# Kernel tuning notes

Measured on AMD Instinct MI355X. Metric: run time of the kernel, lower is better.

Reference implementation:

```python
import jax, jax.numpy as jnp
import numpy as np

B, N, D_IN, D, E, HEADS = 64, 512, 33, 32, 8192, 4
L, K_HOP, FF = 2, 2, 64  # num_layers, k_hop, dim_feedforward=2*d_out


def setup_inputs():
    key = jax.random.key(0)
    ks = iter(jax.random.split(key, 40))
    def nrm(shape, s=0.05):
        return jax.random.normal(next(ks), shape, jnp.float32) * s
    return {
        "H": jax.random.normal(next(ks), (B, N, D_IN), jnp.float32),
        "edge_index": jax.random.randint(next(ks), (2, E), 0, N, jnp.int32),
        # ObsEmbedding: Linear(33,32) ReLU Linear(32,32) ReLU LayerNorm(32)
        "emb_W1": nrm((D_IN, 32)), "emb_b1": jnp.zeros((32,), jnp.float32),
        "emb_W2": nrm((32, 32)), "emb_b2": jnp.zeros((32,), jnp.float32),
        "emb_ln_g": jnp.ones((32,), jnp.float32), "emb_ln_b": jnp.zeros((32,), jnp.float32),
        # per transformer layer: k_hop PNA-style GNN structure extractor
        # each hop: concat(self, mean, max, sum) -> Linear(4D, D), ReLU
        "gnn_W": nrm((L, K_HOP, 4 * D, D)), "gnn_b": jnp.zeros((L, K_HOP, D), jnp.float32),
        # structure-aware attention: Q,K from GNN-extracted features, V from x
        "Wq": nrm((L, D, D)), "Wk": nrm((L, D, D)), "Wv": nrm((L, D, D)), "Wo": nrm((L, D, D)),
        "bn1_g": jnp.ones((L, D), jnp.float32), "bn1_b": jnp.zeros((L, D), jnp.float32),
        "ff_W1": nrm((L, D, FF)), "ff_b1": jnp.zeros((L, FF), jnp.float32),
        "ff_W2": nrm((L, FF, D)), "ff_b2": jnp.zeros((L, D), jnp.float32),
        "bn2_g": jnp.ones((L, D), jnp.float32), "bn2_b": jnp.zeros((L, D), jnp.float32),
        # final node-level head Linear(d_model, num_class=d_out)
        "out_W": nrm((D, D)), "out_b": jnp.zeros((D,), jnp.float32),
    }


def _ln(x, g, b):
    m = x.mean(-1, keepdims=True)
    v = x.var(-1, keepdims=True)
    return (x - m) * jax.lax.rsqrt(v + 1e-5) * g + b


def _bn(x, g, b):  # batch_norm over all nodes of all graphs (training-mode stats)
    m = x.mean((0, 1))
    v = x.var((0, 1))
    return (x - m) * jax.lax.rsqrt(v + 1e-5) * g + b


def reference(H, edge_index, emb_W1, emb_b1, emb_W2, emb_b2, emb_ln_g, emb_ln_b,
              gnn_W, gnn_b, Wq, Wk, Wv, Wo, bn1_g, bn1_b,
              ff_W1, ff_b1, ff_W2, ff_b2, bn2_g, bn2_b, out_W, out_b):
    src, dst = edge_index[0], edge_index[1]
    # ObsEmbedding
    x = jax.nn.relu(H @ emb_W1 + emb_b1)
    x = jax.nn.relu(x @ emb_W2 + emb_b2)
    x = _ln(x, emb_ln_g, emb_ln_b)  # [B,N,D]
    cnt = jnp.zeros((N, 1), x.dtype).at[dst].add(1.0)  # in-degree, shared across batch
    dh = D // HEADS
    inv_sqrt_dh = np.float32(1.0 / np.sqrt(dh))
    for l in range(L):
        # --- k-hop structure extractor (PNA-style multi-aggregator message passing) ---
        h = x
        for k in range(K_HOP):
            msg = h[:, src]                                   # [B,E,D] gather
            s = jnp.zeros_like(h).at[:, dst].add(msg)         # sum aggregate
            mean = s / jnp.maximum(cnt, 1.0)
            mx = jnp.full_like(h, -1e30).at[:, dst].max(msg)  # max aggregate
            mx = jnp.where(cnt > 0, mx, 0.0)
            h = jax.nn.relu(jnp.concatenate([h, mean, mx, s], -1) @ gnn_W[l, k] + gnn_b[l, k])
        # --- structure-aware multi-head attention (full attention within graph) ---
        q = (h @ Wq[l]).reshape(B, N, HEADS, dh)
        kk = (h @ Wk[l]).reshape(B, N, HEADS, dh)
        v = (x @ Wv[l]).reshape(B, N, HEADS, dh)
        att = jax.nn.softmax(jnp.einsum("bqhd,bkhd->bhqk", q, kk) * inv_sqrt_dh, axis=-1)
        o = jnp.einsum("bhqk,bkhd->bqhd", att, v).reshape(B, N, D) @ Wo[l]
        x = _bn(x + o, bn1_g[l], bn1_b[l])
        f = jax.nn.relu(x @ ff_W1[l] + ff_b1[l]) @ ff_W2[l] + ff_b2[l]
        x = _bn(x + f, bn2_g[l], bn2_b[l])
    return x @ out_W + out_b  # [B,N,d_out], eval mode so dropout is identity
```

## Files before the change

kernel.cpp:

```cpp
#include <hip/hip_runtime.h>
#include <hip/hip_bf16.h>

#define BB 64
#define NN 512
#define DIN 33
#define DD 32
#define EE 8192
#define NHEADS 4
#define DH 8
#define FFD 64

typedef __attribute__((ext_vector_type(4))) float f32x4;
typedef __attribute__((ext_vector_type(4))) short bf16x4;

static __device__ __forceinline__ short f2bf(float x) {
    unsigned u = __float_as_uint(x);
    u = (u + 0x7FFFu + ((u >> 16) & 1u)) >> 16;
    return (short)u;
}

static __device__ __forceinline__ unsigned pack_trunc(float a, float b) {
    return (__float_as_uint(a) >> 16) | (__float_as_uint(b) & 0xFFFF0000u);
}

static __device__ __forceinline__ void mfma16(f32x4& d, bf16x4 a, bf16x4 b) {
#if __has_builtin(__builtin_amdgcn_mfma_f32_16x16x16bf16_1k)
    d = __builtin_amdgcn_mfma_f32_16x16x16bf16_1k(a, b, d, 0, 0, 0);
#else
    asm volatile("s_nop 1\n\tv_mfma_f32_16x16x16_bf16 %0, %1, %2, %0\n\ts_nop 7"
                 : "+v"(d) : "v"(a), "v"(b));
#endif
}

__global__ __launch_bounds__(512) void k_csr(const int* __restrict__ ei,
                                             float* __restrict__ cnt_f,
                                             int* __restrict__ csr_off,
                                             int* __restrict__ csr_src,
                                             float* __restrict__ stats) {
    __shared__ int cnt_s[NN];
    __shared__ int wsum[8];
    int tid = threadIdx.x;
    cnt_s[tid] = 0;
    if (tid < 256) stats[tid] = 0.f;
    __syncthreads();
    const int* src = ei;
    const int* dst = ei + EE;
    for (int e = tid; e < EE; e += 512) atomicAdd(&cnt_s[dst[e]], 1);
    __syncthreads();
    int c = cnt_s[tid];
    int lane = tid & 63, w = tid >> 6;
    int sc_ = c;
    #pragma unroll
    for (int off = 1; off < 64; off <<= 1) {
        int nv = __shfl_up(sc_, off, 64);
        if (lane >= off) sc_ += nv;
    }
    if (lane == 63) wsum[w] = sc_;
    __syncthreads();
    if (tid == 0) {
        int a = 0;
        #pragma unroll
        for (int i = 0; i < 8; ++i) { int t = wsum[i]; wsum[i] = a; a += t; }
    }
    __syncthreads();
    int excl = sc_ - c + wsum[w];
    cnt_f[tid] = (float)c;
    csr_off[tid] = excl;
    if (tid == 511) csr_off[NN] = excl + c;
    __syncthreads();
    cnt_s[tid] = excl;
    __syncthreads();
    for (int e = tid; e < EE; e += 512) {
        int d = dst[e];
        int p = atomicAdd(&cnt_s[d], 1);
        csr_src[p] = src[e];
    }
}

__global__ __launch_bounds__(256) void k_emb(const float* __restrict__ H,
                                             const float* __restrict__ W1, const float* __restrict__ b1,
                                             const float* __restrict__ W2, const float* __restrict__ b2,
                                             const float* __restrict__ g,  const float* __restrict__ be,
                                             float* __restrict__ xb, float* __restrict__ xt) {
    __shared__ float sW1[DIN * DD];
    __shared__ float sW2[DD * DD];
    __shared__ float sb1[DD], sb2[DD], sg[DD], sbe[DD];
    __shared__ float sin_[8][DIN + 3];
    int tid = threadIdx.x;
    for (int i = tid; i < DIN * DD; i += 256) sW1[i] = W1[i];
    for (int i = tid; i < DD * DD; i += 256) sW2[i] = W2[i];
    if (tid < DD) { sb1[tid] = b1[tid]; sb2[tid] = b2[tid]; sg[tid] = g[tid]; sbe[tid] = be[tid]; }
    int grp = tid >> 5, lane = tid & 31;
    size_t node = (size_t)blockIdx.x * 8 + grp;
    const float* hrow = H + node * DIN;
    sin_[grp][lane] = hrow[lane];
    if (lane == 0) sin_[grp][32] = hrow[32];
    __syncthreads();
    float acc = sb1[lane];
    #pragma unroll
    for (int i = 0; i < DIN; ++i) acc += sin_[grp][i] * sW1[i * DD + lane];
    acc = fmaxf(acc, 0.f);
    float acc2 = sb2[lane];
    #pragma unroll
    for (int i = 0; i < DD; ++i) acc2 += __shfl(acc, i, 32) * sW2[i * DD + lane];
    acc2 = fmaxf(acc2, 0.f);
    float s = acc2;
    for (int off = 16; off; off >>= 1) s += __shfl_xor(s, off, 32);
    float m = s * (1.f / 32.f);
    float dv = acc2 - m;
    float sq = dv * dv;
    for (int off = 16; off; off >>= 1) sq += __shfl_xor(sq, off, 32);
    float var = sq * (1.f / 32.f);
    float v = dv * rsqrtf(var + 1e-5f) * sg[lane] + sbe[lane];
    xb[node * DD + lane] = v;
    int b = (int)(node >> 9), n = (int)(node & 511);
    xt[(size_t)n * 2048 + b * DD + lane] = v;
}

__global__ __launch_bounds__(256) void k_gnn1(const float* __restrict__ src, float* __restrict__ ht,
                                              const float* __restrict__ cnt_f,
                                              const int* __restrict__ csr_off,
                                              const int* __restrict__ csr_src,
                                              const float* __restrict__ W, const float* __restrict__ bias,
                                              const float* __restrict__ bnstats,
                                              const float* __restrict__ bng, const float* __restrict__ bnb) {
    __shared__ short conc[32 * 132];
    __shared__ short sWt[32 * 132];
    __shared__ float sb[DD];
    __shared__ float scv[DD], offv[DD];
    int tid = threadIdx.x;
    int n = blockIdx.x >> 1, half = blockIdx.x & 1;
    for (int i = tid; i < 128 * DD; i += 256) {
        int k = i >> 5, d = i & 31;
        sWt[d * 132 + k] = f2bf(W[i]);
    }
    if (tid < DD) {
        sb[tid] = bias[tid];
        if (bnstats) {
            float mean = bnstats[tid] * (1.f / 32768.f);
            float var  = bnstats[DD + tid] * (1.f / 32768.f) - mean * mean;
            float sc = rsqrtf(var + 1e-5f) * bng[tid];
            scv[tid] = sc; offv[tid] = bnb[tid] - mean * sc;
        } else { scv[tid] = 1.f; offv[tid] = 0.f; }
    }
    __syncthreads();
    float4 sc4, of4;
    { int d0 = (tid * 4) & 31;
      sc4.x = scv[d0]; sc4.y = scv[d0 + 1]; sc4.z = scv[d0 + 2]; sc4.w = scv[d0 + 3];
      of4.x = offv[d0]; of4.y = offv[d0 + 1]; of4.z = offv[d0 + 2]; of4.w = offv[d0 + 3]; }
    const float* xbase = src + (size_t)half * 1024 + tid * 4;
    float4 hv = *(const float4*)&xbase[(size_t)n * 2048];
    hv.x = fmaf(hv.x, sc4.x, of4.x); hv.y = fmaf(hv.y, sc4.y, of4.y);
    hv.z = fmaf(hv.z, sc4.z, of4.z); hv.w = fmaf(hv.w, sc4.w, of4.w);
    float4 s = {0.f, 0.f, 0.f, 0.f};
    float4 mx = {-1e30f, -1e30f, -1e30f, -1e30f};
    int beg = csr_off[n], end = csr_off[n + 1];
    int idx = beg;
    for (; idx + 3 < end; idx += 4) {
        int s0 = csr_src[idx], s1 = csr_src[idx + 1], s2 = csr_src[idx + 2], s3 = csr_src[idx + 3];
        float4 v0 = *(const float4*)&xbase[(size_t)s0 * 2048];
        float4 v1 = *(const float4*)&xbase[(size_t)s1 * 2048];
        float4 v2 = *(const float4*)&xbase[(size_t)s2 * 2048];
        float4 v3 = *(const float4*)&xbase[(size_t)s3 * 2048];
        v0.x = fmaf(v0.x, sc4.x, of4.x); v0.y = fmaf(v0.y, sc4.y, of4.y);
        v0.z = fmaf(v0.z, sc4.z, of4.z); v0.w = fmaf(v0.w, sc4.w, of4.w);
        v1.x = fmaf(v1.x, sc4.x, of4.x); v1.y = fmaf(v1.y, sc4.y, of4.y);
        v1.z = fmaf(v1.z, sc4.z, of4.z); v1.w = fmaf(v1.w, sc4.w, of4.w);
        v2.x = fmaf(v2.x, sc4.x, of4.x); v2.y = fmaf(v2.y, sc4.y, of4.y);
        v2.z = fmaf(v2.z, sc4.z, of4.z); v2.w = fmaf(v2.w, sc4.w, of4.w);
        v3.x = fmaf(v3.x, sc4.x, of4.x); v3.y = fmaf(v3.y, sc4.y, of4.y);
        v3.z = fmaf(v3.z, sc4.z, of4.z); v3.w = fmaf(v3.w, sc4.w, of4.w);
        s.x += (v0.x + v1.x) + (v2.x + v3.x);
        s.y += (v0.y + v1.y) + (v2.y + v3.y);
        s.z += (v0.z + v1.z) + (v2.z + v3.z);
        s.w += (v0.w + v1.w) + (v2.w + v3.w);
        mx.x = fmaxf(fmaxf(mx.x, v0.x), fmaxf(v1.x, fmaxf(v2.x, v3.x)));
        mx.y = fmaxf(fmaxf(mx.y, v0.y), fmaxf(v1.y, fmaxf(v2.y, v3.y)));
        mx.z = fmaxf(fmaxf(mx.z, v0.z), fmaxf(v1.z, fmaxf(v2.z, v3.z)));
        mx.w = fmaxf(fmaxf(mx.w, v0.w), fmaxf(v1.w, fmaxf(v2.w, v3.w)));
    }
    for (; idx < end; ++idx) {
        int s0 = csr_src[idx];
        float4 v0 = *(const float4*)&xbase[(size_t)s0 * 2048];
        v0.x = fmaf(v0.x, sc4.x, of4.x); v0.y = fmaf(v0.y, sc4.y, of4.y);
        v0.z = fmaf(v0.z, sc4.z, of4.z); v0.w = fmaf(v0.w, sc4.w, of4.w);
        s.x += v0.x; s.y += v0.y; s.z += v0.z; s.w += v0.w;
        mx.x = fmaxf(mx.x, v0.x); mx.y = fmaxf(mx.y, v0.y);
        mx.z = fmaxf(mx.z, v0.z); mx.w = fmaxf(mx.w, v0.w);
    }
    float c = cnt_f[n];
    float rinv = 1.f / fmaxf(c, 1.f);
    if (!(c > 0.f)) { mx.x = 0.f; mx.y = 0.f; mx.z = 0.f; mx.w = 0.f; }
    int bl = tid >> 3, d0 = (tid & 7) * 4;
    short* cp = &conc[bl * 132];
    bf16x4 t;
    t.x = f2bf(hv.x); t.y = f2bf(hv.y); t.z = f2bf(hv.z); t.w = f2bf(hv.w);
    *(bf16x4*)&cp[d0] = t;
    t.x = f2bf(s.x * rinv); t.y = f2bf(s.y * rinv); t.z = f2bf(s.z * rinv); t.w = f2bf(s.w * rinv);
    *(bf16x4*)&cp[32 + d0] = t;
    t.x = f2bf(mx.x); t.y = f2bf(mx.y); t.z = f2bf(mx.z); t.w = f2bf(mx.w);
    *(bf16x4*)&cp[64 + d0] = t;
    t.x = f2bf(s.x); t.y = f2bf(s.y); t.z = f2bf(s.z); t.w = f2bf(s.w);
    *(bf16x4*)&cp[96 + d0] = t;
    __syncthreads();
    int wid = tid >> 6, lane = tid & 63;
    int cc = lane & 15, g = lane >> 4;
    int arow = (wid >> 1) * 16 + cc;
    int bcol = (wid & 1) * 16 + cc;
    f32x4 acc = {0.f, 0.f, 0.f, 0.f};
    #pragma unroll
    for (int ks = 0; ks < 8; ++ks) {
        bf16x4 af = *(const bf16x4*)&conc[arow * 132 + ks * 16 + g * 4];
        bf16x4 bfr = *(const bf16x4*)&sWt[bcol * 132 + ks * 16 + g * 4];
        mfma16(acc, af, bfr);
    }
    float bia = sb[bcol];
    int brow = (wid >> 1) * 16 + g * 4;
    float* obase = &ht[(size_t)n * 2048 + half * 1024 + bcol];
    #pragma unroll
    for (int r = 0; r < 4; ++r) {
        obase[(size_t)(brow + r) * DD] = fmaxf(acc[r] + bia, 0.f);
    }
}

__global__ __launch_bounds__(256) void k_gnn2(const float* __restrict__ hsrc,
                                              const float* __restrict__ cnt_f,
                                              const int* __restrict__ csr_off,
                                              const int* __restrict__ csr_src,
                                              const float* __restrict__ W, const float* __restrict__ bias,
                                              const float* __restrict__ xsrc,
                                              const float* __restrict__ bnstats,
                                              const float* __restrict__ bng, const float* __restrict__ bnb,
                                              const float* __restrict__ Wq, const float* __restrict__ Wk,
                                              const float* __restrict__ Wv,
                                              short* __restrict__ qb2, short* __restrict__ kb2,
                                              short* __restrict__ vb2) {
    __shared__ short conc[32 * 132];
    __shared__ short sWt[32 * 132];
    __shared__ short sWqT[32 * 36], sWkT[32 * 36], sWvT[32 * 36];
    __shared__ short h_lds[32 * 36], x_lds[32 * 36];
    __shared__ float sb[DD];
    __shared__ float scv[DD], offv[DD];
    int tid = threadIdx.x;
    int n = blockIdx.x >> 1, half = blockIdx.x & 1;
    for (int i = tid; i < 128 * DD; i += 256) {
        int k = i >> 5, d = i & 31;
        sWt[d * 132 + k] = f2bf(W[i]);
    }
    {
        const float isq = 0.35355339059327373f;
        for (int i = tid; i < 1024; i += 256) {
            int k = i >> 5, col = i & 31;
            sWqT[col * 36 + k] = f2bf(Wq[i] * isq);
            sWkT[col * 36 + k] = f2bf(Wk[i]);
            sWvT[col * 36 + k] = f2bf(Wv[i]);
        }
    }
    if (tid < DD) {
        sb[tid] = bias[tid];
        if (bnstats) {
            float mean = bnstats[tid] * (1.f / 32768.f);
            float var  = bnstats[DD + tid] * (1.f / 32768.f) - mean * mean;
            float sc = rsqrtf(var + 1e-5f) * bng[tid];
            scv[tid] = sc; offv[tid] = bnb[tid] - mean * sc;
        } else { scv[tid] = 1.f; offv[tid] = 0.f; }
    }
    __syncthreads();
    {
        int bl = tid >> 3, d0 = (tid & 7) * 4;
        float4 x4 = *(const float4*)&xsrc[(size_t)n * 2048 + half * 1024 + bl * 32 + d0];
        x4.x = fmaf(x4.x, scv[d0], offv[d0]);
        x4.y = fmaf(x4.y, scv[d0 + 1], offv[d0 + 1]);
        x4.z = fmaf(x4.z, scv[d0 + 2], offv[d0 + 2]);
        x4.w = fmaf(x4.w, scv[d0 + 3], offv[d0 + 3]);
        bf16x4 xp; xp.x = f2bf(x4.x); xp.y = f2bf(x4.y); xp.z = f2bf(x4.z); xp.w = f2bf(x4.w);
        *(bf16x4*)&x_lds[bl * 36 + d0] = xp;
    }
    const float* xbase = hsrc + (size_t)half * 1024 + tid * 4;
    float4 hv = *(const float4*)&xbase[(size_t)n * 2048];
    float4 s = {0.f, 0.f, 0.f, 0.f};
    float4 mx = {-1e30f, -1e30f, -1e30f, -1e30f};
    int beg = csr_off[n], end = csr_off[n + 1];
    int idx = beg;
    for (; idx + 3 < end; idx += 4) {
        int s0 = csr_src[idx], s1 = csr_src[idx + 1], s2 = csr_src[idx + 2], s3 = csr_src[idx + 3];
        float4 v0 = *(const float4*)&xbase[(size_t)s0 * 2048];
        float4 v1 = *(const float4*)&xbase[(size_t)s1 * 2048];
        float4 v2 = *(const float4*)&xbase[(size_t)s2 * 2048];
        float4 v3 = *(const float4*)&xbase[(size_t)s3 * 2048];
        s.x += (v0.x + v1.x) + (v2.x + v3.x);
        s.y += (v0.y + v1.y) + (v2.y + v3.y);
        s.z += (v0.z + v1.z) + (v2.z + v3.z);
        s.w += (v0.w + v1.w) + (v2.w + v3.w);
        mx.x = fmaxf(fmaxf(mx.x, v0.x), fmaxf(v1.x, fmaxf(v2.x, v3.x)));
        mx.y = fmaxf(fmaxf(mx.y, v0.y), fmaxf(v1.y, fmaxf(v2.y, v3.y)));
        mx.z = fmaxf(fmaxf(mx.z, v0.z), fmaxf(v1.z, fmaxf(v2.z, v3.z)));
        mx.w = fmaxf(fmaxf(mx.w, v0.w), fmaxf(v1.w, fmaxf(v2.w, v3.w)));
    }
    for (; idx < end; ++idx) {
        int s0 = csr_src[idx];
        float4 v0 = *(const float4*)&xbase[(size_t)s0 * 2048];
        s.x += v0.x; s.y += v0.y; s.z += v0.z; s.w += v0.w;
        mx.x = fmaxf(mx.x, v0.x); mx.y = fmaxf(mx.y, v0.y);
        mx.z = fmaxf(mx.z, v0.z); mx.w = fmaxf(mx.w, v0.w);
    }
    float c = cnt_f[n];
    float rinv = 1.f / fmaxf(c, 1.f);
    if (!(c > 0.f)) { mx.x = 0.f; mx.y = 0.f; mx.z = 0.f; mx.w = 0.f; }
    int bl = tid >> 3, d0 = (tid & 7) * 4;
    short* cp = &conc[bl * 132];
    bf16x4 t;
    t.x = f2bf(hv.x); t.y = f2bf(hv.y); t.z = f2bf(hv.z); t.w = f2bf(hv.w);
    *(bf16x4*)&cp[d0] = t;
    t.x = f2bf(s.x * rinv); t.y = f2bf(s.y * rinv); t.z = f2bf(s.z * rinv); t.w = f2bf(s.w * rinv);
    *(bf16x4*)&cp[32 + d0] = t;
    t.x = f2bf(mx.x); t.y = f2bf(mx.y); t.z = f2bf(mx.z); t.w = f2bf(mx.w);
    *(bf16x4*)&cp[64 + d0] = t;
    t.x = f2bf(s.x); t.y = f2bf(s.y); t.z = f2bf(s.z); t.w = f2bf(s.w);
    *(bf16x4*)&cp[96 + d0] = t;
    __syncthreads();
    int wid = tid >> 6, lane = tid & 63;
    int cc = lane & 15, g = lane >> 4;
    int arow = (wid >> 1) * 16 + cc;
    int bcol = (wid & 1) * 16 + cc;
    f32x4 acc = {0.f, 0.f, 0.f, 0.f};
    #pragma unroll
    for (int ks = 0; ks < 8; ++ks) {
        bf16x4 af = *(const bf16x4*)&conc[arow * 132 + ks * 16 + g * 4];
        bf16x4 bfr = *(const bf16x4*)&sWt[bcol * 132 + ks * 16 + g * 4];
        mfma16(acc, af, bfr);
    }
    float bia = sb[bcol];
    int brow = (wid >> 1) * 16 + g * 4;
    #pragma unroll
    for (int r = 0; r < 4; ++r) {
        h_lds[(brow + r) * 36 + bcol] = f2bf(fmaxf(acc[r] + bia, 0.f));
    }
    __syncthreads();
    int tr = wid >> 1, tc = wid & 1;
    f32x4 qa = {0.f, 0.f, 0.f, 0.f}, ka = qa, va = qa;
    #pragma unroll
    for (int ks = 0; ks < 2; ++ks) {
        bf16x4 ha = *(const bf16x4*)&h_lds[(tr * 16 + cc) * 36 + ks * 16 + g * 4];
        bf16x4 xa = *(const bf16x4*)&x_lds[(tr * 16 + cc) * 36 + ks * 16 + g * 4];
        bf16x4 wq = *(const bf16x4*)&sWqT[(tc * 16 + cc) * 36 + ks * 16 + g * 4];
        bf16x4 wk = *(const bf16x4*)&sWkT[(tc * 16 + cc) * 36 + ks * 16 + g * 4];
        bf16x4 wv = *(const bf16x4*)&sWvT[(tc * 16 + cc) * 36 + ks * 16 + g * 4];
        mfma16(qa, ha, wq);
        mfma16(ka, ha, wk);
        mfma16(va, xa, wv);
    }
    int dcol = tc * 16 + cc;
    size_t base = ((size_t)(half * 32 + tr * 16 + g * 4) * NN + n) * DD + dcol;
    #pragma unroll
    for (int r = 0; r < 4; ++r) {
        size_t p = base + (size_t)r * (NN * DD);
        qb2[p] = f2bf(qa[r]);
        kb2[p] = f2bf(ka[r]);
        vb2[p] = f2bf(va[r]);
    }
}

__global__ __launch_bounds__(256) void k_attn_proj(const short* __restrict__ qb2,
                                                   const short* __restrict__ kb2,
                                                   const short* __restrict__ vb2,
                                                   const float* __restrict__ x,
                                                   const float* __restrict__ bnstats,
                                                   const float* __restrict__ bng,
                                                   const float* __restrict__ bnb,
                                                   const float* __restrict__ Wo,
                                                   float* __restrict__ t,
                                                   float* __restrict__ stats) {
    __shared__ short Vt[NHEADS * DH * 528];
    __shared__ short Ot[64 * 36];
    __shared__ short sWoT[DD * 36];
    __shared__ float rs[4][DD], rq[4][DD];
    __shared__ float scv[DD], offv[DD];
    int bid = blockIdx.x;
    int qs = bid & 7, b = bid >> 3;
    int tid = threadIdx.x;

    for (int i = tid; i < 1024; i += 256) {
        int k = i >> 5, col = i & 31;
        sWoT[col * 36 + k] = f2bf(Wo[i]);
    }
    if (tid < DD) {
        if (bnstats) {
            float mean = bnstats[tid] * (1.f / 32768.f);
            float var  = bnstats[DD + tid] * (1.f / 32768.f) - mean * mean;
            float sc = rsqrtf(var + 1e-5f) * bng[tid];
            scv[tid] = sc; offv[tid] = bnb[tid] - mean * sc;
        } else { scv[tid] = 1.f; offv[tid] = 0.f; }
    }
    {
        size_t g0 = ((size_t)b * NN + tid * 2) * DD;
        #pragma unroll
        for (int h2 = 0; h2 < 4; ++h2) {
            uint4 v0 = *(const uint4*)&vb2[g0 + h2 * 8];
            uint4 v1 = *(const uint4*)&vb2[g0 + DD + h2 * 8];
            unsigned* vt = (unsigned*)&Vt[h2 * DH * 528];
            vt[0 * 264 + tid] = (v0.x & 0xFFFFu) | (v1.x << 16);
            vt[1 * 264 + tid] = (v0.x >> 16)     | (v1.x & 0xFFFF0000u);
            vt[2 * 264 + tid] = (v0.y & 0xFFFFu) | (v1.y << 16);
            vt[3 * 264 + tid] = (v0.y >> 16)     | (v1.y & 0xFFFF0000u);
            vt[4 * 264 + tid] = (v0.z & 0xFFFFu) | (v1.z << 16);
            vt[5 * 264 + tid] = (v0.z >> 16)     | (v1.z & 0xFFFF0000u);
            vt[6 * 264 + tid] = (v0.w & 0xFFFFu) | (v1.w << 16);
            vt[7 * 264 + tid] = (v0.w >> 16)     | (v1.w & 0xFFFF0000u);
        }
    }
    __syncthreads();

    int h = tid >> 6, lane = tid & 63;
    int c = lane & 15, g = lane >> 4;
    int c7 = c & 7;
    bf16x4 z4 = {0, 0, 0, 0};
    bf16x4 qf0 = z4, qf1 = z4, qf2 = z4, qf3 = z4;
    if (g < 2) {
        const short* qbase = &qb2[(((size_t)b * NN + qs * 64) * DD) + h * DH + g * 4];
        qf0 = *(const bf16x4*)&qbase[(size_t)(c) * DD];
        qf1 = *(const bf16x4*)&qbase[(size_t)(16 + c) * DD];
        qf2 = *(const bf16x4*)&qbase[(size_t)(32 + c) * DD];
        qf3 = *(const bf16x4*)&qbase[(size_t)(48 + c) * DD];
    }
    const short* kbase = &kb2[((size_t)b * NN) * DD + h * DH + g * 4];
    float l0 = 0.f, l1 = 0.f, l2 = 0.f, l3 = 0.f;
    f32x4 o0 = {0.f, 0.f, 0.f, 0.f}, o1 = o0, o2 = o0, o3 = o0;
    union U { unsigned u[2]; bf16x4 v4; };

    for (int kc = 0; kc < 32; ++kc) {
        bf16x4 kf = z4;
        if (g < 2) kf = *(const bf16x4*)&kbase[(size_t)(kc * 16 + c) * DD];
        bf16x4 vf = z4;
        {
            bf16x4 vl = *(const bf16x4*)&Vt[(h * DH + c7) * 528 + kc * 16 + g * 4];
            if (c < 8) vf = vl;
        }
        f32x4 st0 = {0.f, 0.f, 0.f, 0.f}, st1 = st0, st2 = st0, st3 = st0;
        mfma16(st0, kf, qf0);
        mfma16(st1, kf, qf1);
        mfma16(st2, kf, qf2);
        mfma16(st3, kf, qf3);
        {
            float p0 = __expf(st0[0]), p1 = __expf(st0[1]), p2 = __expf(st0[2]), p3 = __expf(st0[3]);
            l0 += (p0 + p1) + (p2 + p3);
            U pu; pu.u[0] = pack_trunc(p0, p1); pu.u[1] = pack_trunc(p2, p3);
            mfma16(o0, vf, pu.v4);
        }
        {
            float p0 = __expf(st1[0]), p1 = __expf(st1[1]), p2 = __expf(st1[2]), p3 = __expf(st1[3]);
            l1 += (p0 + p1) + (p2 + p3);
            U pu; pu.u[0] = pack_trunc(p0, p1); pu.u[1] = pack_trunc(p2, p3);
            mfma16(o1, vf, pu.v4);
        }
        {
            float p0 = __expf(st2[0]), p1 = __expf(st2[1]), p2 = __expf(st2[2]), p3 = __expf(st2[3]);
            l2 += (p0 + p1) + (p2 + p3);
            U pu; pu.u[0] = pack_trunc(p0, p1); pu.u[1] = pack_trunc(p2, p3);
            mfma16(o2, vf, pu.v4);
        }
        {
            float p0 = __expf(st3[0]), p1 = __expf(st3[1]), p2 = __expf(st3[2]), p3 = __expf(st3[3]);
            l3 += (p0 + p1) + (p2 + p3);
            U pu; pu.u[0] = pack_trunc(p0, p1); pu.u[1] = pack_trunc(p2, p3);
            mfma16(o3, vf, pu.v4);
        }
    }
    l0 += __shfl_xor(l0, 16, 64); l0 += __shfl_xor(l0, 32, 64);
    l1 += __shfl_xor(l1, 16, 64); l1 += __shfl_xor(l1, 32, 64);
    l2 += __shfl_xor(l2, 16, 64); l2 += __shfl_xor(l2, 32, 64);
    l3 += __shfl_xor(l3, 16, 64); l3 += __shfl_xor(l3, 32, 64);
    if (g < 2) {
        float inv0 = 1.f / l0, inv1 = 1.f / l1, inv2 = 1.f / l2, inv3 = 1.f / l3;
        int fb = h * DH + g * 4;
        #pragma unroll
        for (int r = 0; r < 4; ++r) {
            Ot[(c) * 36 + fb + r]      = f2bf(o0[r] * inv0);
            Ot[(16 + c) * 36 + fb + r] = f2bf(o1[r] * inv1);
            Ot[(32 + c) * 36 + fb + r] = f2bf(o2[r] * inv2);
            Ot[(48 + c) * 36 + fb + r] = f2bf(o3[r] * inv3);
        }
    }
    __syncthreads();
    f32x4 pa0 = {0.f, 0.f, 0.f, 0.f}, pa1 = pa0;
    #pragma unroll
    for (int ks = 0; ks < 2; ++ks) {
        bf16x4 af = *(const bf16x4*)&Ot[(h * 16 + c) * 36 + ks * 16 + g * 4];
        bf16x4 b0 = *(const bf16x4*)&sWoT[c * 36 + ks * 16 + g * 4];
        bf16x4 b1 = *(const bf16x4*)&sWoT[(16 + c) * 36 + ks * 16 + g * 4];
        mfma16(pa0, af, b0);
        mfma16(pa1, af, b1);
    }
    float sc0 = scv[c], of0 = offv[c], sc1 = scv[16 + c], of1 = offv[16 + c];
    float ls0 = 0.f, lq0 = 0.f, ls1 = 0.f, lq1 = 0.f;
    size_t rowbase = ((size_t)b * NN + qs * 64 + h * 16 + g * 4) * DD;
    #pragma unroll
    for (int r = 0; r < 4; ++r) {
        float xv0 = fmaf(x[rowbase + (size_t)r * DD + c], sc0, of0);
        float tv0 = xv0 + pa0[r];
        t[rowbase + (size_t)r * DD + c] = tv0;
        ls0 += tv0; lq0 += tv0 * tv0;
        float xv1 = fmaf(x[rowbase + (size_t)r * DD + 16 + c], sc1, of1);
        float tv1 = xv1 + pa1[r];
        t[rowbase + (size_t)r * DD + 16 + c] = tv1;
        ls1 += tv1; lq1 += tv1 * tv1;
    }
    ls0 += __shfl_xor(ls0, 16, 64); ls0 += __shfl_xor(ls0, 32, 64);
    lq0 += __shfl_xor(lq0, 16, 64); lq0 += __shfl_xor(lq0, 32, 64);
    ls1 += __shfl_xor(ls1, 16, 64); ls1 += __shfl_xor(ls1, 32, 64);
    lq1 += __shfl_xor(lq1, 16, 64); lq1 += __shfl_xor(lq1, 32, 64);
    if (g == 0) {
        rs[h][c] = ls0; rs[h][16 + c] = ls1;
        rq[h][c] = lq0; rq[h][16 + c] = lq1;
    }
    __syncthreads();
    if (tid < DD) {
        float a = (rs[0][tid] + rs[1][tid]) + (rs[2][tid] + rs[3][tid]);
        float b2 = (rq[0][tid] + rq[1][tid]) + (rq[2][tid] + rq[3][tid]);
        atomicAdd(&stats[tid], a);
        atomicAdd(&stats[DD + tid], b2);
    }
}

__global__ __launch_bounds__(256) void k_ff(const float* __restrict__ t, const float* __restrict__ stats,
                                            const float* __restrict__ g1, const float* __restrict__ be1,
                                            const float* __restrict__ W1, const float* __restrict__ fb1,
                                            const float* __restrict__ W2, const float* __restrict__ fb2,
                                            float* __restrict__ t2, float* __restrict__ t2n,
                                            float* __restrict__ stats2) {
    __shared__ short x1b[64 * 36];
    __shared__ float x1f[64 * 33];
    __shared__ short hm[64 * 68];
    __shared__ short sW1T[FFD * 36];
    __shared__ short sW2T[DD * 68];
    __shared__ float sc[DD], sm[DD], sbe[DD], sb2v[DD];
    __shared__ float sb1v[FFD];
    __shared__ float rs[4][DD], rq[4][DD];
    int tid = threadIdx.x;
    for (int i = tid; i < 2048; i += 256) {
        int k = i >> 6, col = i & 63;
        sW1T[col * 36 + k] = f2bf(W1[i]);
        int k2 = i >> 5, col2 = i & 31;
        sW2T[col2 * 68 + k2] = f2bf(W2[i]);
    }
    if (tid < DD) {
        float mean = stats[tid] * (1.f / 32768.f);
        float var  = stats[DD + tid] * (1.f / 32768.f) - mean * mean;
        sc[tid] = rsqrtf(var + 1e-5f) * g1[tid];
        sm[tid] = mean; sbe[tid] = be1[tid]; sb2v[tid] = fb2[tid];
    }
    if (tid < FFD) sb1v[tid] = fb1[tid];
    __syncthreads();
    size_t node0 = (size_t)blockIdx.x * 64;
    {
        int row = tid >> 2, cb = (tid & 3) * 8;
        const float* tp = &t[(node0 + row) * DD + cb];
        float4 a = *(const float4*)tp;
        float4 bq = *(const float4*)(tp + 4);
        float v0 = (a.x - sm[cb + 0]) * sc[cb + 0] + sbe[cb + 0];
        float v1 = (a.y - sm[cb + 1]) * sc[cb + 1] + sbe[cb + 1];
        float v2 = (a.z - sm[cb + 2]) * sc[cb + 2] + sbe[cb + 2];
        float v3 = (a.w - sm[cb + 3]) * sc[cb + 3] + sbe[cb + 3];
        float v4 = (bq.x - sm[cb + 4]) * sc[cb + 4] + sbe[cb + 4];
        float v5 = (bq.y - sm[cb + 5]) * sc[cb + 5] + sbe[cb + 5];
        float v6 = (bq.z - sm[cb + 6]) * sc[cb + 6] + sbe[cb + 6];
        float v7 = (bq.w - sm[cb + 7]) * sc[cb + 7] + sbe[cb + 7];
        float* xf = &x1f[row * 33 + cb];
        xf[0] = v0; xf[1] = v1; xf[2] = v2; xf[3] = v3;
        xf[4] = v4; xf[5] = v5; xf[6] = v6; xf[7] = v7;
        bf16x4 p0; p0.x = f2bf(v0); p0.y = f2bf(v1); p0.z = f2bf(v2); p0.w = f2bf(v3);
        bf16x4 p1; p1.x = f2bf(v4); p1.y = f2bf(v5); p1.z = f2bf(v6); p1.w = f2bf(v7);
        *(bf16x4*)&x1b[row * 36 + cb] = p0;
        *(bf16x4*)&x1b[row * 36 + cb + 4] = p1;
    }
    __syncthreads();
    int w = tid >> 6, lane = tid & 63, c = lane & 15, g = lane >> 4;
    f32x4 m0 = {0.f, 0.f, 0.f, 0.f}, m1 = m0, m2 = m0, m3 = m0;
    #pragma unroll
    for (int ks = 0; ks < 2; ++ks) {
        bf16x4 af = *(const bf16x4*)&x1b[(w * 16 + c) * 36 + ks * 16 + g * 4];
        mfma16(m0, af, *(const bf16x4*)&sW1T[(c) * 36 + ks * 16 + g * 4]);
        mfma16(m1, af, *(const bf16x4*)&sW1T[(16 + c) * 36 + ks * 16 + g * 4]);
        mfma16(m2, af, *(const bf16x4*)&sW1T[(32 + c) * 36 + ks * 16 + g * 4]);
        mfma16(m3, af, *(const bf16x4*)&sW1T[(48 + c) * 36 + ks * 16 + g * 4]);
    }
    {
        float b0 = sb1v[c], b1 = sb1v[16 + c], b2 = sb1v[32 + c], b3 = sb1v[48 + c];
        #pragma unroll
        for (int r = 0; r < 4; ++r) {
            short* hr = &hm[(w * 16 + g * 4 + r) * 68];
            hr[c]      = f2bf(fmaxf(m0[r] + b0, 0.f));
            hr[16 + c] = f2bf(fmaxf(m1[r] + b1, 0.f));
            hr[32 + c] = f2bf(fmaxf(m2[r] + b2, 0.f));
            hr[48 + c] = f2bf(fmaxf(m3[r] + b3, 0.f));
        }
    }
    __syncthreads();
    f32x4 f0 = {0.f, 0.f, 0.f, 0.f}, f1 = f0;
    #pragma unroll
    for (int ks = 0; ks < 4; ++ks) {
        bf16x4 af = *(const bf16x4*)&hm[(w * 16 + c) * 68 + ks * 16 + g * 4];
        mfma16(f0, af, *(const bf16x4*)&sW2T[(c) * 68 + ks * 16 + g * 4]);
        mfma16(f1, af, *(const bf16x4*)&sW2T[(16 + c) * 68 + ks * 16 + g * 4]);
    }
    __syncthreads();
    float* t2s = (float*)hm;
    float ls0 = 0.f, lq0 = 0.f, ls1 = 0.f, lq1 = 0.f;
    float bb0 = sb2v[c], bb1 = sb2v[16 + c];
    #pragma unroll
    for (int r = 0; r < 4; ++r) {
        int row = w * 16 + g * 4 + r;
        float tv0 = x1f[row * 33 + c] + f0[r] + bb0;
        t2[(node0 + row) * DD + c] = tv0;
        t2s[row * DD + c] = tv0;
        ls0 += tv0; lq0 += tv0 * tv0;
        float tv1 = x1f[row * 33 + 16 + c] + f1[r] + bb1;
        t2[(node0 + row) * DD + 16 + c] = tv1;
        t2s[row * DD + 16 + c] = tv1;
        ls1 += tv1; lq1 += tv1 * tv1;
    }
    ls0 += __shfl_xor(ls0, 16, 64); ls0 += __shfl_xor(ls0, 32, 64);
    lq0 += __shfl_xor(lq0, 16, 64); lq0 += __shfl_xor(lq0, 32, 64);
    ls1 += __shfl_xor(ls1, 16, 64); ls1 += __shfl_xor(ls1, 32, 64);
    lq1 += __shfl_xor(lq1, 16, 64); lq1 += __shfl_xor(lq1, 32, 64);
    if (g == 0) {
        rs[w][c] = ls0; rs[w][16 + c] = ls1;
        rq[w][c] = lq0; rq[w][16 + c] = lq1;
    }
    __syncthreads();
    if (tid < DD) {
        float a = (rs[0][tid] + rs[1][tid]) + (rs[2][tid] + rs[3][tid]);
        float bsum = (rq[0][tid] + rq[1][tid]) + (rq[2][tid] + rq[3][tid]);
        atomicAdd(&stats2[tid], a);
        atomicAdd(&stats2[DD + tid], bsum);
    }
    if (t2n) {
        int bb = (int)(node0 >> 9), nn0 = (int)(node0 & 511);
        for (int i = tid; i < 512; i += 256) {
            int row = i >> 3, c4 = i & 7;
            float4 v = *(const float4*)&t2s[row * DD + c4 * 4];
            *(float4*)&t2n[(size_t)(nn0 + row) * 2048 + bb * DD + c4 * 4] = v;
        }
    }
}

__global__ __launch_bounds__(256) void k_out(const float* __restrict__ t2, const float* __restrict__ stats,
                                             const float* __restrict__ g2, const float* __restrict__ be2,
                                             const float* __restrict__ outW, const float* __restrict__ outb,
                                             float* __restrict__ out) {
    __shared__ short x1b[64 * 36];
    __shared__ short sWoT[DD * 36];
    __shared__ float scv[DD], offv[DD], sbo[DD];
    int tid = threadIdx.x;
    for (int i = tid; i < 1024; i += 256) {
        int k = i >> 5, col = i & 31;
        sWoT[col * 36 + k] = f2bf(outW[i]);
    }
    if (tid < DD) {
        float mean = stats[tid] * (1.f / 32768.f);
        float var  = stats[DD + tid] * (1.f / 32768.f) - mean * mean;
        float sc = rsqrtf(var + 1e-5f) * g2[tid];
        scv[tid] = sc; offv[tid] = be2[tid] - mean * sc;
        sbo[tid] = outb[tid];
    }
    __syncthreads();
    size_t node0 = (size_t)blockIdx.x * 64;
    {
        int row = tid >> 2, cb = (tid & 3) * 8;
        const float* tp = &t2[(node0 + row) * DD + cb];
        float4 a = *(const float4*)tp;
        float4 bq = *(const float4*)(tp + 4);
        bf16x4 p0, p1;
        p0.x = f2bf(fmaf(a.x, scv[cb + 0], offv[cb + 0]));
        p0.y = f2bf(fmaf(a.y, scv[cb + 1], offv[cb + 1]));
        p0.z = f2bf(fmaf(a.z, scv[cb + 2], offv[cb + 2]));
        p0.w = f2bf(fmaf(a.w, scv[cb + 3], offv[cb + 3]));
        p1.x = f2bf(fmaf(bq.x, scv[cb + 4], offv[cb + 4]));
        p1.y = f2bf(fmaf(bq.y, scv[cb + 5], offv[cb + 5]));
        p1.z = f2bf(fmaf(bq.z, scv[cb + 6], offv[cb + 6]));
        p1.w = f2bf(fmaf(bq.w, scv[cb + 7], offv[cb + 7]));
        *(bf16x4*)&x1b[row * 36 + cb] = p0;
        *(bf16x4*)&x1b[row * 36 + cb + 4] = p1;
    }
    __syncthreads();
    int w = tid >> 6, lane = tid & 63, c = lane & 15, g = lane >> 4;
    f32x4 a0 = {0.f, 0.f, 0.f, 0.f}, a1 = a0;
    #pragma unroll
    for (int ks = 0; ks < 2; ++ks) {
        bf16x4 af = *(const bf16x4*)&x1b[(w * 16 + c) * 36 + ks * 16 + g * 4];
        mfma16(a0, af, *(const bf16x4*)&sWoT[(c) * 36 + ks * 16 + g * 4]);
        mfma16(a1, af, *(const bf16x4*)&sWoT[(16 + c) * 36 + ks * 16 + g * 4]);
    }
    float b0 = sbo[c], b1 = sbo[16 + c];
    #pragma unroll
    for (int r = 0; r < 4; ++r) {
        int row = w * 16 + g * 4 + r;
        out[(node0 + row) * DD + c]      = a0[r] + b0;
        out[(node0 + row) * DD + 16 + c] = a1[r] + b1;
    }
}

extern "C" void kernel_launch(void* const* d_in, const int* in_sizes, int n_in,
                              void* d_out, int out_size, void* d_ws, size_t ws_size,
                              hipStream_t stream) {
    const float* H    = (const float*)d_in[0];
    const int*   ei   = (const int*)  d_in[1];
    const float* eW1  = (const float*)d_in[2];
    const float* eb1  = (const float*)d_in[3];
    const float* eW2  = (const float*)d_in[4];
    const float* eb2  = (const float*)d_in[5];
    const float* elg  = (const float*)d_in[6];
    const float* elb  = (const float*)d_in[7];
    const float* gW   = (const float*)d_in[8];
    const float* gb   = (const float*)d_in[9];
    const float* Wq   = (const float*)d_in[10];
    const float* Wk   = (const float*)d_in[11];
    const float* Wv   = (const float*)d_in[12];
    const float* Wo   = (const float*)d_in[13];
    const float* bn1g = (const float*)d_in[14];
    const float* bn1b = (const float*)d_in[15];
    const float* fW1  = (const float*)d_in[16];
    const float* fb1  = (const float*)d_in[17];
    const float* fW2  = (const float*)d_in[18];
    const float* fb2  = (const float*)d_in[19];
    const float* bn2g = (const float*)d_in[20];
    const float* bn2b = (const float*)d_in[21];
    const float* oW   = (const float*)d_in[22];
    const float* obv  = (const float*)d_in[23];
    float* out = (float*)d_out;

    float* ws = (float*)d_ws;
    const size_t BIGSZ = (size_t)BB * NN * DD;
    float* xb  = ws;
    float* xt  = ws + 1 * BIGSZ;
    float* hA  = ws + 2 * BIGSZ;
    float* hB  = ws + 3 * BIGSZ;
    short* qb2 = (short*)(ws + 4 * BIGSZ);
    short* kb2 = qb2 + BIGSZ;
    short* vb2 = (short*)(ws + 5 * BIGSZ);
    float* t2n = ws + 6 * BIGSZ;
    float* tb  = ws + 7 * BIGSZ;
    float* smalls = ws + 8 * BIGSZ;
    float* cnt_f   = smalls;
    int*   csr_off = (int*)(smalls + 512);
    int*   csr_src = (int*)(smalls + 512 + 516);
    float* stats   = smalls + 512 + 516 + 8192;

    k_csr<<<1, 512, 0, stream>>>(ei, cnt_f, csr_off, csr_src, stats);
    k_emb<<<BB * NN / 8, 256, 0, stream>>>(H, eW1, eb1, eW2, eb2, elg, elb, xb, xt);

    for (int l = 0; l < 2; ++l) {
        const float* gW0 = gW + (size_t)(l * 2 + 0) * 128 * DD;
        const float* gW1 = gW + (size_t)(l * 2 + 1) * 128 * DD;
        const float* gb0 = gb + (size_t)(l * 2 + 0) * DD;
        const float* gb1 = gb + (size_t)(l * 2 + 1) * DD;
        float* st1 = stats + l * 128;
        float* st2 = stats + l * 128 + 64;
        const float* pstats = (l == 0) ? nullptr : stats + 64;
        const float* pg = (l == 0) ? nullptr : bn2g;
        const float* pb = (l == 0) ? nullptr : bn2b;
        const float* gsrc = (l == 0) ? xt : t2n;
        const float* xres = (l == 0) ? xb : hB;

        k_gnn1<<<NN * 2, 256, 0, stream>>>(gsrc, hA, cnt_f, csr_off, csr_src, gW0, gb0,
                                           pstats, pg, pb);
        k_gnn2<<<NN * 2, 256, 0, stream>>>(hA, cnt_f, csr_off, csr_src, gW1, gb1,
                                           gsrc, pstats, pg, pb,
                                           Wq + l * DD * DD, Wk + l * DD * DD, Wv + l * DD * DD,
                                           qb2, kb2, vb2);
        k_attn_proj<<<BB * 8, 256, 0, stream>>>(qb2, kb2, vb2, xres, pstats, pg, pb,
                                                Wo + l * DD * DD, tb, st1);
        k_ff<<<512, 256, 0, stream>>>(tb, st1, bn1g + l * DD, bn1b + l * DD,
                                      fW1 + l * DD * FFD, fb1 + l * FFD,
                                      fW2 + l * FFD * DD, fb2 + l * DD,
                                      hB, (l == 0) ? t2n : nullptr, st2);
    }
    k_out<<<512, 256, 0, stream>>>(hB, stats + 192, bn2g + DD, bn2b + DD, oW, obv, out);
}
```

Measured before the change: 204.6 us.

## Fuse CSR build into embedding kernel, stage K in LDS, defer BN affine

Merges the single-block CSR construction into the embedding launch as an extra block, removing one kernel launch. The GNN gather loops now use 8-wide unrolling, and the batch-norm scale/offset is applied once to the aggregated sum and max rather than to every neighbour. The attention kernel copies K into shared memory and folds log2(e) into the Q scale so it can use exp2f. The extra LDS for K lowers occupancy, and the deferred affine applied to the max is only correct when the BN scale is positive.

```diff
diff --git a/kernel.cpp b/kernel.cpp
--- a/kernel.cpp
+++ b/kernel.cpp
@@ -32,61 +32,62 @@
 #endif
 }
 
-__global__ __launch_bounds__(512) void k_csr(const int* __restrict__ ei,
-                                             float* __restrict__ cnt_f,
-                                             int* __restrict__ csr_off,
-                                             int* __restrict__ csr_src,
-                                             float* __restrict__ stats) {
-    __shared__ int cnt_s[NN];
-    __shared__ int wsum[8];
-    int tid = threadIdx.x;
-    cnt_s[tid] = 0;
-    if (tid < 256) stats[tid] = 0.f;
-    __syncthreads();
-    const int* src = ei;
-    const int* dst = ei + EE;
-    for (int e = tid; e < EE; e += 512) atomicAdd(&cnt_s[dst[e]], 1);
-    __syncthreads();
-    int c = cnt_s[tid];
-    int lane = tid & 63, w = tid >> 6;
-    int sc_ = c;
-    #pragma unroll
-    for (int off = 1; off < 64; off <<= 1) {
-        int nv = __shfl_up(sc_, off, 64);
-        if (lane >= off) sc_ += nv;
-    }
-    if (lane == 63) wsum[w] = sc_;
-    __syncthreads();
-    if (tid == 0) {
-        int a = 0;
-        #pragma unroll
-        for (int i = 0; i < 8; ++i) { int t = wsum[i]; wsum[i] = a; a += t; }
-    }
-    __syncthreads();
-    int excl = sc_ - c + wsum[w];
-    cnt_f[tid] = (float)c;
-    csr_off[tid] = excl;
-    if (tid == 511) csr_off[NN] = excl + c;
-    __syncthreads();
-    cnt_s[tid] = excl;
-    __syncthreads();
-    for (int e = tid; e < EE; e += 512) {
-        int d = dst[e];
-        int p = atomicAdd(&cnt_s[d], 1);
-        csr_src[p] = src[e];
-    }
-}
-
-__global__ __launch_bounds__(256) void k_emb(const float* __restrict__ H,
-                                             const float* __restrict__ W1, const float* __restrict__ b1,
-                                             const float* __restrict__ W2, const float* __restrict__ b2,
-                                             const float* __restrict__ g,  const float* __restrict__ be,
-                                             float* __restrict__ xb, float* __restrict__ xt) {
+__global__ __launch_bounds__(256) void k_embcsr(const float* __restrict__ H,
+                                                const float* __restrict__ W1, const float* __restrict__ b1,
+                                                const float* __restrict__ W2, const float* __restrict__ b2,
+                                                const float* __restrict__ g,  const float* __restrict__ be,
+                                                float* __restrict__ xb, float* __restrict__ xt,
+                                                const int* __restrict__ ei,
+                                                float* __restrict__ cnt_f,
+                                                int* __restrict__ csr_off,
+                                                int* __restrict__ csr_src,
+                                                float* __restrict__ stats) {
     __shared__ float sW1[DIN * DD];
     __shared__ float sW2[DD * DD];
     __shared__ float sb1[DD], sb2[DD], sg[DD], sbe[DD];
     __shared__ float sin_[8][DIN + 3];
+    __shared__ int cnt_s[NN];
+    __shared__ int wsum[4];
     int tid = threadIdx.x;
+    if (blockIdx.x == (BB * NN / 8)) {
+        cnt_s[tid] = 0; cnt_s[tid + 256] = 0;
+        stats[tid] = 0.f;
+        __syncthreads();
+        const int* src = ei;
+        const int* dst = ei + EE;
+        for (int e = tid; e < EE; e += 256) atomicAdd(&cnt_s[dst[e]], 1);
+        __syncthreads();
+        int c0 = cnt_s[2 * tid], c1 = cnt_s[2 * tid + 1];
+        int cp = c0 + c1;
+        int lane = tid & 63, w = tid >> 6;
+        int sc = cp;
+        #pragma unroll
+        for (int off = 1; off < 64; off <<= 1) {
+            int v = __shfl_up(sc, off, 64);
+            if (lane >= off) sc += v;
+        }
+        if (lane == 63) wsum[w] = sc;
+        __syncthreads();
+        if (tid == 0) {
+            int a = 0;
+            #pragma unroll
+            for (int i = 0; i < 4; ++i) { int t = wsum[i]; wsum[i] = a; a += t; }
+        }
+        __syncthreads();
+        int excl = sc - cp + wsum[w];
+        cnt_f[2 * tid] = (float)c0; cnt_f[2 * tid + 1] = (float)c1;
+        csr_off[2 * tid] = excl; csr_off[2 * tid + 1] = excl + c0;
+        if (tid == 255) csr_off[NN] = excl + cp;
+        __syncthreads();
+        cnt_s[2 * tid] = excl; cnt_s[2 * tid + 1] = excl + c0;
+        __syncthreads();
+        for (int e = tid; e < EE; e += 256) {
+            int d = dst[e];
+            int p = atomicAdd(&cnt_s[d], 1);
+            csr_src[p] = src[e];
+        }
+        return;
+    }
     for (int i = tid; i < DIN * DD; i += 256) sW1[i] = W1[i];
     for (int i = tid; i < DD * DD; i += 256) sW2[i] = W2[i];
     if (tid < DD) { sb1[tid] = b1[tid]; sb2[tid] = b2[tid]; sg[tid] = g[tid]; sbe[tid] = be[tid]; }
@@ -150,57 +151,61 @@
       of4.x = offv[d0]; of4.y = offv[d0 + 1]; of4.z = offv[d0 + 2]; of4.w = offv[d0 + 3]; }
     const float* xbase = src + (size_t)half * 1024 + tid * 4;
     float4 hv = *(const float4*)&xbase[(size_t)n * 2048];
-    hv.x = fmaf(hv.x, sc4.x, of4.x); hv.y = fmaf(hv.y, sc4.y, of4.y);
-    hv.z = fmaf(hv.z, sc4.z, of4.z); hv.w = fmaf(hv.w, sc4.w, of4.w);
     float4 s = {0.f, 0.f, 0.f, 0.f};
     float4 mx = {-1e30f, -1e30f, -1e30f, -1e30f};
     int beg = csr_off[n], end = csr_off[n + 1];
     int idx = beg;
+    for (; idx + 7 < end; idx += 8) {
+        float4 v[8];
+        #pragma unroll
+        for (int j = 0; j < 8; ++j)
+            v[j] = *(const float4*)&xbase[(size_t)csr_src[idx + j] * 2048];
+        #pragma unroll
+        for (int j = 0; j < 8; ++j) {
+            s.x += v[j].x; s.y += v[j].y; s.z += v[j].z; s.w += v[j].w;
+            mx.x = fmaxf(mx.x, v[j].x); mx.y = fmaxf(mx.y, v[j].y);
+            mx.z = fmaxf(mx.z, v[j].z); mx.w = fmaxf(mx.w, v[j].w);
+        }
+    }
     for (; idx + 3 < end; idx += 4) {
-        int s0 = csr_src[idx], s1 = csr_src[idx + 1], s2 = csr_src[idx + 2], s3 = csr_src[idx + 3];
-        float4 v0 = *(const float4*)&xbase[(size_t)s0 * 2048];
-        float4 v1 = *(const float4*)&xbase[(size_t)s1 * 2048];
-        float4 v2 = *(const float4*)&xbase[(size_t)s2 * 2048];
-        float4 v3 = *(const float4*)&xbase[(size_t)s3 * 2048];
-        v0.x = fmaf(v0.x, sc4.x, of4.x); v0.y = fmaf(v0.y, sc4.y, of4.y);
-        v0.z = fmaf(v0.z, sc4.z, of4.z); v0.w = fmaf(v0.w, sc4.w, of4.w);
-        v1.x = fmaf(v1.x, sc4.x, of4.x); v1.y = fmaf(v1.y, sc4.y, of4.y);
-        v1.z = fmaf(v1.z, sc4.z, of4.z); v1.w = fmaf(v1.w, sc4.w, of4.w);
-        v2.x = fmaf(v2.x, sc4.x, of4.x); v2.y = fmaf(v2.y, sc4.y, of4.y);
-        v2.z = fmaf(v2.z, sc4.z, of4.z); v2.w = fmaf(v2.w, sc4.w, of4.w);
-        v3.x = fmaf(v3.x, sc4.x, of4.x); v3.y = fmaf(v3.y, sc4.y, of4.y);
-        v3.z = fmaf(v3.z, sc4.z, of4.z); v3.w = fmaf(v3.w, sc4.w, of4.w);
-        s.x += (v0.x + v1.x) + (v2.x + v3.x);
-        s.y += (v0.y + v1.y) + (v2.y + v3.y);
-        s.z += (v0.z + v1.z) + (v2.z + v3.z);
-        s.w += (v0.w + v1.w) + (v2.w + v3.w);
-        mx.x = fmaxf(fmaxf(mx.x, v0.x), fmaxf(v1.x, fmaxf(v2.x, v3.x)));
-        mx.y = fmaxf(fmaxf(mx.y, v0.y), fmaxf(v1.y, fmaxf(v2.y, v3.y)));
-        mx.z = fmaxf(fmaxf(mx.z, v0.z), fmaxf(v1.z, fmaxf(v2.z, v3.z)));
-        mx.w = fmaxf(fmaxf(mx.w, v0.w), fmaxf(v1.w, fmaxf(v2.w, v3.w)));
+        float4 v[4];
+        #pragma unroll
+        for (int j = 0; j < 4; ++j)
+            v[j] = *(const float4*)&xbase[(size_t)csr_src[idx + j] * 2048];
+        #pragma unroll
+        for (int j = 0; j < 4; ++j) {
+            s.x += v[j].x; s.y += v[j].y; s.z += v[j].z; s.w += v[j].w;
+            mx.x = fmaxf(mx.x, v[j].x); mx.y = fmaxf(mx.y, v[j].y);
+            mx.z = fmaxf(mx.z, v[j].z); mx.w = fmaxf(mx.w, v[j].w);
+        }
     }
     for (; idx < end; ++idx) {
-        int s0 = csr_src[idx];
-        float4 v0 = *(const float4*)&xbase[(size_t)s0 * 2048];
-        v0.x = fmaf(v0.x, sc4.x, of4.x); v0.y = fmaf(v0.y, sc4.y, of4.y);
-        v0.z = fmaf(v0.z, sc4.z, of4.z); v0.w = fmaf(v0.w, sc4.w, of4.w);
+        float4 v0 = *(const float4*)&xbase[(size_t)csr_src[idx] * 2048];
         s.x += v0.x; s.y += v0.y; s.z += v0.z; s.w += v0.w;
         mx.x = fmaxf(mx.x, v0.x); mx.y = fmaxf(mx.y, v0.y);
         mx.z = fmaxf(mx.z, v0.z); mx.w = fmaxf(mx.w, v0.w);
     }
     float c = cnt_f[n];
     float rinv = 1.f / fmaxf(c, 1.f);
-    if (!(c > 0.f)) { mx.x = 0.f; mx.y = 0.f; mx.z = 0.f; mx.w = 0.f; }
+    hv.x = fmaf(hv.x, sc4.x, of4.x); hv.y = fmaf(hv.y, sc4.y, of4.y);
+    hv.z = fmaf(hv.z, sc4.z, of4.z); hv.w = fmaf(hv.w, sc4.w, of4.w);
+    float4 sa;
+    sa.x = fmaf(s.x, sc4.x, c * of4.x); sa.y = fmaf(s.y, sc4.y, c * of4.y);
+    sa.z = fmaf(s.z, sc4.z, c * of4.z); sa.w = fmaf(s.w, sc4.w, c * of4.w);
+    if (c > 0.f) {
+        mx.x = fmaf(mx.x, sc4.x, of4.x); mx.y = fmaf(mx.y, sc4.y, of4.y);
+        mx.z = fmaf(mx.z, sc4.z, of4.z); mx.w = fmaf(mx.w, sc4.w, of4.w);
+    } else { mx.x = 0.f; mx.y = 0.f; mx.z = 0.f; mx.w = 0.f; }
     int bl = tid >> 3, d0 = (tid & 7) * 4;
     short* cp = &conc[bl * 132];
     bf16x4 t;
     t.x = f2bf(hv.x); t.y = f2bf(hv.y); t.z = f2bf(hv.z); t.w = f2bf(hv.w);
     *(bf16x4*)&cp[d0] = t;
-    t.x = f2bf(s.x * rinv); t.y = f2bf(s.y * rinv); t.z = f2bf(s.z * rinv); t.w = f2bf(s.w * rinv);
+    t.x = f2bf(sa.x * rinv); t.y = f2bf(sa.y * rinv); t.z = f2bf(sa.z * rinv); t.w = f2bf(sa.w * rinv);
     *(bf16x4*)&cp[32 + d0] = t;
     t.x = f2bf(mx.x); t.y = f2bf(mx.y); t.z = f2bf(mx.z); t.w = f2bf(mx.w);
     *(bf16x4*)&cp[64 + d0] = t;
-    t.x = f2bf(s.x); t.y = f2bf(s.y); t.z = f2bf(s.z); t.w = f2bf(s.w);
+    t.x = f2bf(sa.x); t.y = f2bf(sa.y); t.z = f2bf(sa.z); t.w = f2bf(sa.w);
     *(bf16x4*)&cp[96 + d0] = t;
     __syncthreads();
     int wid = tid >> 6, lane = tid & 63;
@@ -248,10 +253,10 @@
         sWt[d * 132 + k] = f2bf(W[i]);
     }
     {
-        const float isq = 0.35355339059327373f;
+        const float qsc = 0.35355339059327373f * 1.44269504088896f;
         for (int i = tid; i < 1024; i += 256) {
             int k = i >> 5, col = i & 31;
-            sWqT[col * 36 + k] = f2bf(Wq[i] * isq);
+            sWqT[col * 36 + k] = f2bf(Wq[i] * qsc);
             sWkT[col * 36 + k] = f2bf(Wk[i]);
             sWvT[col * 36 + k] = f2bf(Wv[i]);
         }
@@ -282,24 +287,32 @@
     float4 mx = {-1e30f, -1e30f, -1e30f, -1e30f};
     int beg = csr_off[n], end = csr_off[n + 1];
     int idx = beg;
+    for (; idx + 7 < end; idx += 8) {
+        float4 v[8];
+        #pragma unroll
+        for (int j = 0; j < 8; ++j)
+            v[j] = *(const float4*)&xbase[(size_t)csr_src[idx + j] * 2048];
+        #pragma unroll
+        for (int j = 0; j < 8; ++j) {
+            s.x += v[j].x; s.y += v[j].y; s.z += v[j].z; s.w += v[j].w;
+            mx.x = fmaxf(mx.x, v[j].x); mx.y = fmaxf(mx.y, v[j].y);
+            mx.z = fmaxf(mx.z, v[j].z); mx.w = fmaxf(mx.w, v[j].w);
+        }
+    }
     for (; idx + 3 < end; idx += 4) {
-        int s0 = csr_src[idx], s1 = csr_src[idx + 1], s2 = csr_src[idx + 2], s3 = csr_src[idx + 3];
-        float4 v0 = *(const float4*)&xbase[(size_t)s0 * 2048];
-        float4 v1 = *(const float4*)&xbase[(size_t)s1 * 2048];
-        float4 v2 = *(const float4*)&xbase[(size_t)s2 * 2048];
-        float4 v3 = *(const float4*)&xbase[(size_t)s3 * 2048];
-        s.x += (v0.x + v1.x) + (v2.x + v3.x);
-        s.y += (v0.y + v1.y) + (v2.y + v3.y);
-        s.z += (v0.z + v1.z) + (v2.z + v3.z);
-        s.w += (v0.w + v1.w) + (v2.w + v3.w);
-        mx.x = fmaxf(fmaxf(mx.x, v0.x), fmaxf(v1.x, fmaxf(v2.x, v3.x)));
-        mx.y = fmaxf(fmaxf(mx.y, v0.y), fmaxf(v1.y, fmaxf(v2.y, v3.y)));
-        mx.z = fmaxf(fmaxf(mx.z, v0.z), fmaxf(v1.z, fmaxf(v2.z, v3.z)));
-        mx.w = fmaxf(fmaxf(mx.w, v0.w), fmaxf(v1.w, fmaxf(v2.w, v3.w)));
+        float4 v[4];
+        #pragma unroll
+        for (int j = 0; j < 4; ++j)
+            v[j] = *(const float4*)&xbase[(size_t)csr_src[idx + j] * 2048];
+        #pragma unroll
+        for (int j = 0; j < 4; ++j) {
+            s.x += v[j].x; s.y += v[j].y; s.z += v[j].z; s.w += v[j].w;
+            mx.x = fmaxf(mx.x, v[j].x); mx.y = fmaxf(mx.y, v[j].y);
+            mx.z = fmaxf(mx.z, v[j].z); mx.w = fmaxf(mx.w, v[j].w);
+        }
     }
     for (; idx < end; ++idx) {
-        int s0 = csr_src[idx];
-        float4 v0 = *(const float4*)&xbase[(size_t)s0 * 2048];
+        float4 v0 = *(const float4*)&xbase[(size_t)csr_src[idx] * 2048];
         s.x += v0.x; s.y += v0.y; s.z += v0.z; s.w += v0.w;
         mx.x = fmaxf(mx.x, v0.x); mx.y = fmaxf(mx.y, v0.y);
         mx.z = fmaxf(mx.z, v0.z); mx.w = fmaxf(mx.w, v0.w);
@@ -371,6 +384,7 @@
                                                    const float* __restrict__ Wo,
                                                    float* __restrict__ t,
                                                    float* __restrict__ stats) {
+    __shared__ short Ks[NHEADS * NN * DH];
     __shared__ short Vt[NHEADS * DH * 528];
     __shared__ short Ot[64 * 36];
     __shared__ short sWoT[DD * 36];
@@ -391,6 +405,11 @@
             float sc = rsqrtf(var + 1e-5f) * bng[tid];
             scv[tid] = sc; offv[tid] = bnb[tid] - mean * sc;
         } else { scv[tid] = 1.f; offv[tid] = 0.f; }
+    }
+    for (int i = tid; i < 2048; i += 256) {
+        int h2 = i >> 9, r = i & 511;
+        *(uint4*)&Ks[(h2 * NN + r) * DH] =
+            *(const uint4*)&kb2[((size_t)b * NN + r) * DD + h2 * DH];
     }
     {
         size_t g0 = ((size_t)b * NN + tid * 2) * DD;
@@ -423,14 +442,14 @@
         qf2 = *(const bf16x4*)&qbase[(size_t)(32 + c) * DD];
         qf3 = *(const bf16x4*)&qbase[(size_t)(48 + c) * DD];
     }
-    const short* kbase = &kb2[((size_t)b * NN) * DD + h * DH + g * 4];
+    const short* klds = &Ks[(size_t)h * NN * DH + g * 4];
     float l0 = 0.f, l1 = 0.f, l2 = 0.f, l3 = 0.f;
     f32x4 o0 = {0.f, 0.f, 0.f, 0.f}, o1 = o0, o2 = o0, o3 = o0;
     union U { unsigned u[2]; bf16x4 v4; };
 
     for (int kc = 0; kc < 32; ++kc) {
         bf16x4 kf = z4;
-        if (g < 2) kf = *(const bf16x4*)&kbase[(size_t)(kc * 16 + c) * DD];
+        if (g < 2) kf = *(const bf16x4*)&klds[(kc * 16 + c) * DH];
         bf16x4 vf = z4;
         {
             bf16x4 vl = *(const bf16x4*)&Vt[(h * DH + c7) * 528 + kc * 16 + g * 4];
@@ -442,25 +461,25 @@
         mfma16(st2, kf, qf2);
         mfma16(st3, kf, qf3);
         {
-            float p0 = __expf(st0[0]), p1 = __expf(st0[1]), p2 = __expf(st0[2]), p3 = __expf(st0[3]);
+            float p0 = exp2f(st0[0]), p1 = exp2f(st0[1]), p2 = exp2f(st0[2]), p3 = exp2f(st0[3]);
             l0 += (p0 + p1) + (p2 + p3);
             U pu; pu.u[0] = pack_trunc(p0, p1); pu.u[1] = pack_trunc(p2, p3);
             mfma16(o0, vf, pu.v4);
         }
         {
-            float p0 = __expf(st1[0]), p1 = __expf(st1[1]), p2 = __expf(st1[2]), p3 = __expf(st1[3]);
+            float p0 = exp2f(st1[0]), p1 = exp2f(st1[1]), p2 = exp2f(st1[2]), p3 = exp2f(st1[3]);
             l1 += (p0 + p1) + (p2 + p3);
             U pu; pu.u[0] = pack_trunc(p0, p1); pu.u[1] = pack_trunc(p2, p3);
             mfma16(o1, vf, pu.v4);
         }
         {
-            float p0 = __expf(st2[0]), p1 = __expf(st2[1]), p2 = __expf(st2[2]), p3 = __expf(st2[3]);
+            float p0 = exp2f(st2[0]), p1 = exp2f(st2[1]), p2 = exp2f(st2[2]), p3 = exp2f(st2[3]);
             l2 += (p0 + p1) + (p2 + p3);
             U pu; pu.u[0] = pack_trunc(p0, p1); pu.u[1] = pack_trunc(p2, p3);
             mfma16(o2, vf, pu.v4);
         }
         {
-            float p0 = __expf(st3[0]), p1 = __expf(st3[1]), p2 = __expf(st3[2]), p3 = __expf(st3[3]);
+            float p0 = exp2f(st3[0]), p1 = exp2f(st3[1]), p2 = exp2f(st3[2]), p3 = exp2f(st3[3]);
             l3 += (p0 + p1) + (p2 + p3);
             U pu; pu.u[0] = pack_trunc(p0, p1); pu.u[1] = pack_trunc(p2, p3);
             mfma16(o3, vf, pu.v4);
@@ -746,8 +765,8 @@
     int*   csr_src = (int*)(smalls + 512 + 516);
     float* stats   = smalls + 512 + 516 + 8192;
 
-    k_csr<<<1, 512, 0, stream>>>(ei, cnt_f, csr_off, csr_src, stats);
-    k_emb<<<BB * NN / 8, 256, 0, stream>>>(H, eW1, eb1, eW2, eb2, elg, elb, xb, xt);
+    k_embcsr<<<BB * NN / 8 + 1, 256, 0, stream>>>(H, eW1, eb1, eW2, eb2, elg, elb, xb, xt,
+                                                  ei, cnt_f, csr_off, csr_src, stats);
 
     for (int l = 0; l < 2; ++l) {
         const float* gW0 = gW + (size_t)(l * 2 + 0) * 128 * DD;
```

Measured after the change: 206.9 us. Within noise of the previous version (+1.1%).
